# Performance work log

Hardware: AMD Instinct MI355X
Metric: run time of the kernel (lower is better)

## Reference

```python
import jax, jax.numpy as jnp
import numpy as np

EMB = 768  # SentenceT5 embedding dim; MLP input is 2*EMB


def setup_inputs() -> dict:
    key = jax.random.key(0)
    ks = jax.random.split(key, 9)
    B, S, D = 32, 32, 64
    num_doc = jax.random.randint(ks[0], (B,), 8, D + 1, dtype=jnp.int32)
    num_doc = num_doc.at[0].set(D)  # ensure max == padded dim (tf.reduce_max semantics)
    num_seg = jax.random.randint(ks[1], (B,), 4, S + 1, dtype=jnp.int32)
    num_seg = num_seg.at[0].set(S)
    doc_emb = jax.random.normal(ks[2], (B, D, EMB), jnp.float32)
    sum_emb = jax.random.normal(ks[3], (B, S, EMB), jnp.float32)
    # ragged .to_tensor() -> zero rows beyond per-sample length
    doc_emb = doc_emb * (jnp.arange(D)[None, :, None] < num_doc[:, None, None])
    sum_emb = sum_emb * (jnp.arange(S)[None, :, None] < num_seg[:, None, None])
    target_agg = jax.random.uniform(ks[4], (B,), jnp.float32)
    target_inst = jax.random.uniform(ks[5], (B, S), jnp.float32)
    w = lambda k, i, o: jax.random.normal(k, (i, o), jnp.float32) * 0.02
    W1 = w(ks[6], 2 * EMB, EMB)
    b1 = jnp.zeros((EMB,), jnp.float32)
    W2 = w(ks[7], EMB, EMB // 2)
    b2 = jnp.zeros((EMB // 2,), jnp.float32)
    W3 = w(ks[8], EMB // 2, 1)
    b3 = jnp.zeros((1,), jnp.float32)
    return dict(doc_emb=doc_emb, sum_emb=sum_emb, num_document_splits=num_doc,
                num_summary_segments=num_seg, target_agg_score=target_agg,
                target_instance_score=target_inst,
                W1=W1, b1=b1, W2=W2, b2=b2, W3=W3, b3=b3)


def _forward(doc_emb, sum_emb, num_doc, num_seg, W1, b1, W2, b2, W3, b3):
    B, D, E = doc_emb.shape
    S = sum_emb.shape[1]
    # concat([doc, seg]) @ W1 == doc @ W1[:E] + seg @ W1[E:]  (avoids materializing [B,S,D,2E])
    h_doc = jnp.einsum('bde,eh->bdh', doc_emb, W1[:E])   # [B,D,E]
    h_seg = jnp.einsum('bse,eh->bsh', sum_emb, W1[E:])   # [B,S,E]
    h1 = jax.nn.gelu(h_doc[:, None, :, :] + h_seg[:, :, None, :] + b1, approximate=False)  # [B,S,D,E]
    h2 = jax.nn.gelu(jnp.einsum('bsdh,hk->bsdk', h1, W2) + b2, approximate=False)          # [B,S,D,E/2]
    score = jax.nn.sigmoid(jnp.einsum('bsdk,ko->bsdo', h2, W3) + b3)[..., 0]               # [B,S,D]
    mask_d = (jnp.arange(D)[None, :] < num_doc[:, None]).astype(jnp.float32)               # [B,D]
    seg_max = jnp.max(mask_d[:, None, :] * score, axis=-1)                                 # [B,S]
    seg_w = jnp.where(num_seg > 10, 1.0, 100.0).astype(jnp.float32)                        # [B]
    pred = seg_w[:, None] * seg_max                                                        # [B,S]
    # cosine similarity prior (keras CosineSimilarity returns -cos)
    dn = doc_emb * jax.lax.rsqrt(jnp.maximum(jnp.sum(doc_emb * doc_emb, -1, keepdims=True), 1e-12))
    sn = sum_emb * jax.lax.rsqrt(jnp.maximum(jnp.sum(sum_emb * sum_emb, -1, keepdims=True), 1e-12))
    cs = -jnp.einsum('bde,bse->bsd', dn, sn)                                               # [B,S,D]
    dscos = jnp.max(mask_d[:, None, :] * (1.0 + cs) * 0.5, axis=-1)                        # [B,S]
    seg_mask = (jnp.arange(S)[None, :] < num_seg[:, None]).astype(jnp.float32)             # [B,S]
    diff = jnp.abs(dscos - pred) * seg_mask
    cos_prior = jnp.mean(jnp.sum(diff, axis=1) / num_seg.astype(jnp.float32))
    return pred, cos_prior


def reference(doc_emb, sum_emb, num_document_splits, num_summary_segments,
              target_agg_score, target_instance_score,
              W1, b1, W2, b2, W3, b3):
    B, S = target_instance_score.shape
    seg_mask = jnp.arange(S)[None, :] < num_summary_segments[:, None]
    # pad target instance scores with ones beyond per-sample length
    target_instance = jnp.where(seg_mask, target_instance_score, 1.0)
    pred, cos_prior = _forward(doc_emb, sum_emb, num_document_splits, num_summary_segments,
                               W1, b1, W2, b2, W3, b3)
    return (target_agg_score, target_instance, pred, num_summary_segments, cos_prior)
```

## Files before the change

### kernel.cpp

```cpp
#include <hip/hip_runtime.h>
#include <hip/hip_bf16.h>
#include <math.h>


typedef __bf16 bf16x8 __attribute__((ext_vector_type(8)));
typedef float f32x4 __attribute__((ext_vector_type(4)));

__device__ __forceinline__ unsigned short f2bf(float x) {
    unsigned int u = __float_as_uint(x);
    u = (u + 0x7fffu + ((u >> 16) & 1u)) >> 16;
    return (unsigned short)u;
}
__device__ __forceinline__ float exp2_fast(float x) {
    float r; asm("v_exp_f32 %0, %1" : "=v"(r) : "v"(x)); return r;
}
__device__ __forceinline__ float rcp_fast(float x) {
    float r; asm("v_rcp_f32 %0, %1" : "=v"(r) : "v"(x)); return r;
}
__device__ __forceinline__ unsigned int cvt_pk_bf16(float lo, float hi) {
    unsigned int r; asm("v_cvt_pk_bf16_f32 %0, %1, %2" : "=v"(r) : "v"(lo), "v"(hi)); return r;
}
__device__ __forceinline__ float gelu_fast(float x) {
    float t = x * fmaf(x * x, -0.10294325f, -2.3022081f);
    return x * rcp_fast(1.0f + exp2_fast(t));
}
__device__ __forceinline__ float sigmoid_fast(float x) {
    return rcp_fast(1.0f + exp2_fast(x * -1.4426950408889634f));
}
__device__ __forceinline__ float wave_sum(float v) {
    for (int o = 32; o; o >>= 1) v += __shfl_xor(v, o);
    return v;
}
__device__ __forceinline__ float wave_max(float v) {
    for (int o = 32; o; o >>= 1) v = fmaxf(v, __shfl_xor(v, o));
    return v;
}
__device__ __forceinline__ void soft_barrier() {
    __builtin_amdgcn_sched_barrier(0);
    asm volatile("s_waitcnt lgkmcnt(0)" ::: "memory");
    __builtin_amdgcn_s_barrier();
    __builtin_amdgcn_sched_barrier(0);
}
#define GLOAD_LDS16(GP, LP)                                                     \
    __builtin_amdgcn_global_load_lds(                                           \
        (const __attribute__((address_space(1))) unsigned int*)(GP),            \
        (__attribute__((address_space(3))) unsigned int*)(LP), 16, 0, 0)

__global__ __launch_bounds__(256) void prep_all(const float* __restrict__ W1,
                                                const float* __restrict__ W2,
                                                const float* __restrict__ doc,
                                                const float* __restrict__ sume,
                                                unsigned short* __restrict__ W1t,
                                                unsigned short* __restrict__ W2f,
                                                unsigned short* __restrict__ dnbf,
                                                unsigned short* __restrict__ snbf) {
    __shared__ __align__(16) char shbuf[49152];
    int id = blockIdx.x;
    int t = threadIdx.x;
    if (id < 288) {
        float (*tile)[65] = (float(*)[65])shbuf;
        int bx = id % 12, by = id / 12;
        int r0 = by * 64, c0 = bx * 64;
        #pragma unroll
        for (int p = 0; p < 16; ++p) {
            int r = p * 4 + (t >> 6), c = t & 63;
            tile[r][c] = W1[(r0 + r) * 768 + c0 + c];
        }
        __syncthreads();
        #pragma unroll
        for (int p = 0; p < 16; ++p) {
            int cc = p * 4 + (t >> 6), rr = t & 63;
            W1t[(c0 + cc) * 1536 + r0 + rr] = f2bf(tile[rr][cc]);
        }
    } else if (id < 300) {
        unsigned short* sh = (unsigned short*)shbuf;
        int kt = id - 288;
        #pragma unroll
        for (int p = 0; p < 96; ++p) {
            int u = p * 256 + t;
            int k = u / 384, n = u - k * 384;
            sh[u] = f2bf(W2[(kt * 64 + k) * 384 + n]);
        }
        __syncthreads();
        #pragma unroll
        for (int p = 0; p < 12; ++p) {
            int u = p * 256 + t;
            int lane = u & 63;
            int g = u >> 6;
            int ks = g / 24, fc = g - ks * 24;
            unsigned short tmp[8];
            #pragma unroll
            for (int j = 0; j < 8; ++j)
                tmp[j] = sh[(ks * 32 + (lane >> 4) * 8 + j) * 384 + fc * 16 + (lane & 15)];
            int ktks = kt * 2 + ks;
            *(uint4*)(W2f + ((ktks * 24 + fc) * 64 + lane) * 8) = *(uint4*)tmp;
        }
    } else {
        int row = (id - 300) * 4 + (t >> 6);
        int lane = t & 63;
        const float* p; unsigned short* dst;
        if (row < 2048) { p = doc + row * 768; dst = dnbf + row * 768; }
        else            { p = sume + (row - 2048) * 768; dst = snbf + (row - 2048) * 768; }
        const float* pp = p + lane * 12;
        float4 a0 = *(const float4*)(pp);
        float4 a1 = *(const float4*)(pp + 4);
        float4 a2 = *(const float4*)(pp + 8);
        float s = a0.x*a0.x + a0.y*a0.y + a0.z*a0.z + a0.w*a0.w
                + a1.x*a1.x + a1.y*a1.y + a1.z*a1.z + a1.w*a1.w
                + a2.x*a2.x + a2.y*a2.y + a2.z*a2.z + a2.w*a2.w;
        s = wave_sum(s);
        float r = rsqrtf(fmaxf(s, 1e-12f));
        unsigned short* dd = dst + lane * 12;
        dd[0]  = f2bf(a0.x * r); dd[1]  = f2bf(a0.y * r);
        dd[2]  = f2bf(a0.z * r); dd[3]  = f2bf(a0.w * r);
        dd[4]  = f2bf(a1.x * r); dd[5]  = f2bf(a1.y * r);
        dd[6]  = f2bf(a1.z * r); dd[7]  = f2bf(a1.w * r);
        dd[8]  = f2bf(a2.x * r); dd[9]  = f2bf(a2.y * r);
        dd[10] = f2bf(a2.z * r); dd[11] = f2bf(a2.w * r);
    }
}

__global__ __launch_bounds__(256) void gemm1(const float* __restrict__ doc,
                                             const float* __restrict__ sume,
                                             const unsigned short* __restrict__ W1t,
                                             const float* __restrict__ b1,
                                             unsigned short* __restrict__ hd,
                                             unsigned short* __restrict__ hs) {
    __shared__ __align__(16) unsigned short Asw[2][128 * 64];
    __shared__ __align__(16) unsigned short Bsw[2][64 * 64];
    int t = threadIdx.x;
    int row0 = blockIdx.y * 128, col0 = blockIdx.x * 64;
    bool is_doc = row0 < 2048;
    const float* A = is_doc ? (doc + row0 * 768) : (sume + (row0 - 2048) * 768);
    int kbase = is_doc ? 0 : 768;
    unsigned short* O = is_doc ? (hd + row0 * 768) : (hs + (row0 - 2048) * 768);

    int l = t & 63, w = t >> 6;
    int wr = w >> 1, wc = w & 1;
    int srow = t >> 3, sko = (t & 7) * 8;
    f32x4 acc[4][2];
    #pragma unroll
    for (int i = 0; i < 4; ++i)
        #pragma unroll
        for (int j = 0; j < 2; ++j) acc[i][j] = (f32x4)0.f;

    float4 fA0[4], fA1[4];
    bf16x8 bB[2];

#define G_LOAD(KT)                                                              \
    {                                                                           \
        _Pragma("unroll")                                                       \
        for (int p = 0; p < 4; ++p) {                                           \
            fA0[p] = *(const float4*)(A + (p * 32 + srow) * 768 + (KT) + sko);  \
            fA1[p] = *(const float4*)(A + (p * 32 + srow) * 768 + (KT) + sko + 4); \
        }                                                                       \
        _Pragma("unroll")                                                       \
        for (int p = 0; p < 2; ++p)                                             \
            bB[p] = *(const bf16x8*)(W1t + (col0 + p * 32 + srow) * 1536 + kbase + (KT) + sko); \
    }

#define G_STORE(BUF)                                                            \
    {                                                                           \
        char* AB = (char*)Asw[BUF];                                             \
        char* BB = (char*)Bsw[BUF];                                             \
        _Pragma("unroll")                                                       \
        for (int p = 0; p < 4; ++p) {                                           \
            uint4 v = make_uint4(cvt_pk_bf16(fA0[p].x, fA0[p].y),               \
                                 cvt_pk_bf16(fA0[p].z, fA0[p].w),               \
                                 cvt_pk_bf16(fA1[p].x, fA1[p].y),               \
                                 cvt_pk_bf16(fA1[p].z, fA1[p].w));              \
            int r = p * 32 + srow;                                              \
            int byte = (r * 128 + sko * 2) ^ ((r & 7) << 4);                    \
            *(uint4*)(AB + byte) = v;                                           \
        }                                                                       \
        _Pragma("unroll")                                                       \
        for (int p = 0; p < 2; ++p) {                                           \
            int r = p * 32 + srow;                                              \
            int byte = (r * 128 + sko * 2) ^ ((r & 7) << 4);                    \
            *(bf16x8*)(BB + byte) = bB[p];                                      \
        }                                                                       \
    }

    G_LOAD(0)
    G_STORE(0)
    G_LOAD(64)
    soft_barrier();

    #pragma unroll 1
    for (int i = 0; i < 12; ++i) {
        int cur = i & 1;
        const char* AR = (const char*)Asw[cur];
        const char* BR = (const char*)Bsw[cur];
        #pragma unroll
        for (int ks = 0; ks < 2; ++ks) {
            int koff = (ks * 32 + (l >> 4) * 8) * 2;
            bf16x8 af[4], bfr[2];
            #pragma unroll
            for (int fr = 0; fr < 4; ++fr) {
                int r = wr * 64 + fr * 16 + (l & 15);
                af[fr] = *(const bf16x8*)(AR + ((r * 128 + koff) ^ ((r & 7) << 4)));
            }
            #pragma unroll
            for (int fc = 0; fc < 2; ++fc) {
                int n = wc * 32 + fc * 16 + (l & 15);
                bfr[fc] = *(const bf16x8*)(BR + ((n * 128 + koff) ^ ((n & 7) << 4)));
            }
            #pragma unroll
            for (int fr = 0; fr < 4; ++fr)
                #pragma unroll
                for (int fc = 0; fc < 2; ++fc)
                    acc[fr][fc] = __builtin_amdgcn_mfma_f32_16x16x32_bf16(af[fr], bfr[fc], acc[fr][fc], 0, 0, 0);
        }
        if (i < 11) {
            G_STORE(cur ^ 1)
            if (i < 10) G_LOAD((i + 2) * 64)
        }
        soft_barrier();
    }
#undef G_LOAD
#undef G_STORE

    #pragma unroll
    for (int fr = 0; fr < 4; ++fr)
        #pragma unroll
        for (int fc = 0; fc < 2; ++fc) {
            int c = col0 + wc * 32 + fc * 16 + (l & 15);
            float badd = is_doc ? 0.0f : b1[c];
            #pragma unroll
            for (int j = 0; j < 4; ++j) {
                int r = wr * 64 + fr * 16 + (l >> 4) * 4 + j;
                O[r * 768 + c] = f2bf(acc[fr][fc][j] + badd);
            }
        }
}

__global__ __launch_bounds__(512) void score_mfma(
    const unsigned short* __restrict__ hd, const unsigned short* __restrict__ hs,
    const unsigned short* __restrict__ W2f,
    const float* __restrict__ b2, const float* __restrict__ W3,
    const float* __restrict__ b3, const int* __restrict__ ndoc,
    const int* __restrict__ nseg, const unsigned short* __restrict__ dnbf,
    const unsigned short* __restrict__ snbf, float* __restrict__ out,
    float* __restrict__ dscos)
{
    __shared__ __align__(16) char smem[90112];
    float* spart = (float*)smem;
    float* sred  = (float*)smem;

    int t = threadIdx.x;
    int l = t & 63, w = t >> 6;

    if (blockIdx.x < 32) {
        int b = (int)blockIdx.x;
        if (w < 4) {
            const unsigned short* sb = snbf + b * 32 * 768;
            const unsigned short* db = dnbf + b * 64 * 768;
            int arow = l & 15, ak = (l >> 4) * 8;
            int d0 = w * 16;
            f32x4 acc0 = (f32x4)0.f, acc1 = (f32x4)0.f;
            #pragma unroll
            for (int k = 0; k < 768; k += 32) {
                bf16x8 a0 = *(const bf16x8*)(sb + arow * 768 + k + ak);
                bf16x8 a1 = *(const bf16x8*)(sb + (16 + arow) * 768 + k + ak);
                bf16x8 bb = *(const bf16x8*)(db + (d0 + arow) * 768 + k + ak);
                acc0 = __builtin_amdgcn_mfma_f32_16x16x32_bf16(a0, bb, acc0, 0, 0, 0);
                acc1 = __builtin_amdgcn_mfma_f32_16x16x32_bf16(a1, bb, acc1, 0, 0, 0);
            }
            int nd = ndoc[b];
            int d = d0 + (l & 15);
            float v0[4], v1[4];
            #pragma unroll
            for (int j = 0; j < 4; ++j) {
                v0[j] = (d < nd) ? (1.f - acc0[j]) * 0.5f : 0.f;
                v1[j] = (d < nd) ? (1.f - acc1[j]) * 0.5f : 0.f;
            }
            #pragma unroll
            for (int o = 1; o < 16; o <<= 1) {
                #pragma unroll
                for (int j = 0; j < 4; ++j) {
                    v0[j] = fmaxf(v0[j], __shfl_xor(v0[j], o));
                    v1[j] = fmaxf(v1[j], __shfl_xor(v1[j], o));
                }
            }
            if ((l & 15) == 0) {
                int srw = (l >> 4) * 4;
                #pragma unroll
                for (int j = 0; j < 4; ++j) {
                    sred[w * 32 + srw + j] = v0[j];
                    sred[w * 32 + 16 + srw + j] = v1[j];
                }
            }
        }
        __syncthreads();
        if (t < 32)
            dscos[(int)blockIdx.x * 32 + t] = fmaxf(fmaxf(sred[t], sred[32 + t]),
                                                    fmaxf(sred[64 + t], sred[96 + t]));
        return;
    }

    int sb = (int)blockIdx.x - 32;
    int lb = (sb & 7) * 64 + (sb >> 3);
    int b = lb >> 4, sp = lb & 15;
    int s0 = sp * 2;
    int nd = ndoc[b], ns = nseg[b];
    int wr = w >> 2, wc = w & 3;

    f32x4 acc[4][6];
    #pragma unroll
    for (int i = 0; i < 4; ++i)
        #pragma unroll
        for (int j = 0; j < 6; ++j) acc[i][j] = (f32x4)0.f;

    int r = t >> 2;
    int k8 = t & 3;
    int d = r & 63, sl = r >> 6;
    const unsigned short* hdp = hd + (b * 64 + d) * 768 + k8 * 8;
    const unsigned short* hsp = hs + (b * 32 + s0 + sl) * 768 + k8 * 8;
    int abyte = ((r >> 4) * 1024 + k8 * 256 + (r & 15) * 16) ^ (k8 << 4);

    bf16x8 hdA, hsA, hdB, hsB;

#define A_LOAD(KT, HD8, HS8)                                                    \
    {                                                                           \
        HD8 = *(const bf16x8*)(hdp + (KT));                                     \
        HS8 = *(const bf16x8*)(hsp + (KT));                                     \
    }

#define B_STAGE(KC, BUF)                                                        \
    {                                                                           \
        _Pragma("unroll")                                                       \
        for (int q = 0; q < 3; ++q) {                                           \
            int fc = w * 3 + q;                                                 \
            const unsigned short* gsrc = W2f + (((KC) * 24 + fc) * 64 + l) * 8; \
            GLOAD_LDS16(gsrc, smem + 16384 + (BUF) * 24576 + fc * 1024);        \
        }                                                                       \
    }

#define A_STORE(HD8, HS8, BUF)                                                  \
    {                                                                           \
        const unsigned int* hu = (const unsigned int*)&HD8;                     \
        const unsigned int* su = (const unsigned int*)&HS8;                     \
        unsigned int au[4];                                                     \
        _Pragma("unroll")                                                       \
        for (int e = 0; e < 4; ++e) {                                           \
            float x0 = __uint_as_float(hu[e] << 16) + __uint_as_float(su[e] << 16); \
            float x1 = __uint_as_float(hu[e] & 0xffff0000u) + __uint_as_float(su[e] & 0xffff0000u); \
            au[e] = cvt_pk_bf16(gelu_fast(x0), gelu_fast(x1));                  \
        }                                                                       \
        *(uint4*)(smem + (BUF) * 8192 + abyte) = make_uint4(au[0], au[1], au[2], au[3]); \
    }

#define MFMA_PHASE(ABUF, BBUF)                                                  \
    {                                                                           \
        const char* AR = (const char*)smem + (ABUF) * 8192;                     \
        const char* BR = (const char*)smem + 16384 + (BBUF) * 24576;            \
        __builtin_amdgcn_s_setprio(1);                                          \
        bf16x8 af[4];                                                           \
        _Pragma("unroll")                                                       \
        for (int fr = 0; fr < 4; ++fr)                                          \
            af[fr] = *(const bf16x8*)(AR + (wr * 4 + fr) * 1024                 \
                                         + ((l * 16) ^ ((l >> 4) << 4)));       \
        _Pragma("unroll")                                                       \
        for (int i2 = 0; i2 < 6; ++i2) {                                        \
            bf16x8 bq = *(const bf16x8*)(BR + (wc * 6 + i2) * 1024 + l * 16);   \
            _Pragma("unroll")                                                   \
            for (int fr = 0; fr < 4; ++fr)                                      \
                acc[fr][i2] = __builtin_amdgcn_mfma_f32_16x16x32_bf16(af[fr], bq, acc[fr][i2], 0, 0, 0); \
        }                                                                       \
        __builtin_amdgcn_s_setprio(0);                                          \
    }

#define SYNC_CNT()                                                              \
    __builtin_amdgcn_sched_barrier(0);                                          \
    asm volatile("s_waitcnt vmcnt(5) lgkmcnt(0)" ::: "memory");                 \
    __builtin_amdgcn_s_barrier();                                               \
    __builtin_amdgcn_sched_barrier(0);

#define K_ITER(J, HDL, HSL, HDS, HSS)                                           \
    {                                                                           \
        int i_ = base + (J);                                                    \
        if (i_ < 22) {                                                          \
            B_STAGE(i_ + 2, ((J) + 2) % 3)                                      \
            A_LOAD((i_ + 2) * 32, HDL, HSL)                                     \
        }                                                                       \
        MFMA_PHASE((J) & 1, (J) % 3)                                            \
        if (i_ < 23) A_STORE(HDS, HSS, ((J) + 1) & 1)                           \
        SYNC_CNT()                                                              \
    }

    A_LOAD(0, hdA, hsA)
    B_STAGE(0, 0)
    B_STAGE(1, 1)
    A_STORE(hdA, hsA, 0)
    A_LOAD(32, hdB, hsB)
    SYNC_CNT()

    #pragma unroll 1
    for (int base = 0; base < 24; base += 6) {
        K_ITER(0, hdA, hsA, hdB, hsB)
        K_ITER(1, hdB, hsB, hdA, hsA)
        K_ITER(2, hdA, hsA, hdB, hsB)
        K_ITER(3, hdB, hsB, hdA, hsA)
        K_ITER(4, hdA, hsA, hdB, hsB)
        K_ITER(5, hdB, hsB, hdA, hsA)
    }
#undef A_LOAD
#undef B_STAGE
#undef A_STORE
#undef MFMA_PHASE
#undef SYNC_CNT
#undef K_ITER

    float b2v[6], w3v[6];
    #pragma unroll
    for (int i2 = 0; i2 < 6; ++i2) {
        int col = wc * 96 + i2 * 16 + (l & 15);
        b2v[i2] = b2[col];
        w3v[i2] = W3[col];
    }
    __syncthreads();
    #pragma unroll
    for (int fr = 0; fr < 4; ++fr) {
        #pragma unroll
        for (int j = 0; j < 4; ++j) {
            float pr = 0.f;
            #pragma unroll
            for (int i2 = 0; i2 < 6; ++i2)
                pr += gelu_fast(acc[fr][i2][j] + b2v[i2]) * w3v[i2];
            pr += __shfl_xor(pr, 1);
            pr += __shfl_xor(pr, 2);
            pr += __shfl_xor(pr, 4);
            pr += __shfl_xor(pr, 8);
            if ((l & 15) == 0)
                spart[wc * 128 + wr * 64 + fr * 16 + (l >> 4) * 4 + j] = pr;
        }
    }
    __syncthreads();
    if (t < 128) {
        int row = t;
        float v = spart[row] + spart[128 + row] + spart[256 + row] + spart[384 + row] + b3[0];
        float sc = sigmoid_fast(v);
        int dd = row & 63, sl2 = row >> 6;
        float m = (dd < nd) ? sc : 0.f;
        m = wave_max(m);
        if ((t & 63) == 0) {
            float segw = (ns > 10) ? 1.f : 100.f;
            out[1056 + b * 32 + s0 + sl2] = segw * m;
        }
    }
}

__global__ __launch_bounds__(1024) void finish_k(const float* __restrict__ agg,
                                                 const float* __restrict__ tinst,
                                                 const int* __restrict__ nseg,
                                                 const float* __restrict__ dscos,
                                                 float* __restrict__ out) {
    __shared__ float red[16];
    int t = threadIdx.x, lane = t & 63, w = t >> 6;
    int b = t >> 5, s = t & 31;
    int ns = nseg[b];
    out[32 + t] = (s < ns) ? tinst[t] : 1.0f;
    if (t < 32) {
        out[t] = agg[t];
        out[2080 + t] = (float)nseg[t];
    }
    float pred = out[1056 + t];
    float v = (s < ns) ? fabsf(dscos[t] - pred) / (float)ns : 0.f;
    v = wave_sum(v);
    if (lane == 0) red[w] = v;
    __syncthreads();
    if (w == 0) {
        float x = (lane < 16) ? red[lane] : 0.f;
        x = wave_sum(x);
        if (lane == 0) out[2112] = x * (1.f / 32.f);
    }
}

extern "C" void kernel_launch(void* const* d_in, const int* in_sizes, int n_in,
                              void* d_out, int out_size, void* d_ws, size_t ws_size,
                              hipStream_t stream) {
    const float* doc   = (const float*)d_in[0];
    const float* sume  = (const float*)d_in[1];
    const int*   ndoc  = (const int*)d_in[2];
    const int*   nseg  = (const int*)d_in[3];
    const float* agg   = (const float*)d_in[4];
    const float* tinst = (const float*)d_in[5];
    const float* W1    = (const float*)d_in[6];
    const float* b1    = (const float*)d_in[7];
    const float* W2    = (const float*)d_in[8];
    const float* b2    = (const float*)d_in[9];
    const float* W3    = (const float*)d_in[10];
    const float* b3    = (const float*)d_in[11];
    float* out = (float*)d_out;
    char* ws = (char*)d_ws;

    unsigned short* hd   = (unsigned short*)(ws);
    unsigned short* hs   = (unsigned short*)(ws + 3145728);
    unsigned short* W1t  = (unsigned short*)(ws + 4718592);
    unsigned short* W2f  = (unsigned short*)(ws + 7077888);
    unsigned short* dnbf = (unsigned short*)(ws + 7667712);
    unsigned short* snbf = (unsigned short*)(ws + 10813440);
    float* dscos = (float*)(ws + 12386304);

    prep_all<<<1068, 256, 0, stream>>>(W1, W2, doc, sume, W1t, W2f, dnbf, snbf);
    gemm1<<<dim3(12, 24), 256, 0, stream>>>(doc, sume, W1t, b1, hd, hs);
    score_mfma<<<544, 512, 0, stream>>>(hd, hs, W2f, b2, W3, b3, ndoc, nseg,
                                        dnbf, snbf, out, dscos);
    finish_k<<<1, 1024, 0, stream>>>(agg, tinst, nseg, dscos, out);
}
```

Measured before the change: 99.20 us.

## Shrink score tile to one segment per 256-thread block and peel loop tail

The score kernel now uses 256-thread blocks that each handle a single (batch, segment) pair over 64 doc rows, instead of 512-thread blocks covering two segments, which doubles the grid to 1056 blocks. Each wave now covers 96 output columns for all 64 rows, so each block stages twice as much W2 per wave with a smaller A tile. The K loop drops its per-iteration bounds checks by peeling the last iterations into an explicit epilogue, and the wait count changes to match. The smaller LDS footprint could let more blocks share a CU, but W2 is reloaded from global memory per segment, twice as often as before, which raises memory traffic.

```diff
diff --git a/kernel.cpp b/kernel.cpp
--- a/kernel.cpp
+++ b/kernel.cpp
@@ -234,7 +234,7 @@
         }
 }
 
-__global__ __launch_bounds__(512) void score_mfma(
+__global__ __launch_bounds__(256) void score_mfma(
     const unsigned short* __restrict__ hd, const unsigned short* __restrict__ hs,
     const unsigned short* __restrict__ W2f,
     const float* __restrict__ b2, const float* __restrict__ W3,
@@ -243,7 +243,7 @@
     const unsigned short* __restrict__ snbf, float* __restrict__ out,
     float* __restrict__ dscos)
 {
-    __shared__ __align__(16) char smem[90112];
+    __shared__ __align__(16) char smem[81920];
     float* spart = (float*)smem;
     float* sred  = (float*)smem;
 
@@ -252,7 +252,7 @@
 
     if (blockIdx.x < 32) {
         int b = (int)blockIdx.x;
-        if (w < 4) {
+        {
             const unsigned short* sb = snbf + b * 32 * 768;
             const unsigned short* db = dnbf + b * 64 * 768;
             int arow = l & 15, ak = (l >> 4) * 8;
@@ -299,11 +299,9 @@
     }
 
     int sb = (int)blockIdx.x - 32;
-    int lb = (sb & 7) * 64 + (sb >> 3);
-    int b = lb >> 4, sp = lb & 15;
-    int s0 = sp * 2;
+    int lb = (sb & 7) * 128 + (sb >> 3);
+    int b = lb >> 5, s = lb & 31;
     int nd = ndoc[b], ns = nseg[b];
-    int wr = w >> 2, wc = w & 3;
 
     f32x4 acc[4][6];
     #pragma unroll
@@ -311,12 +309,11 @@
         #pragma unroll
         for (int j = 0; j < 6; ++j) acc[i][j] = (f32x4)0.f;
 
-    int r = t >> 2;
+    int d = t >> 2;
     int k8 = t & 3;
-    int d = r & 63, sl = r >> 6;
     const unsigned short* hdp = hd + (b * 64 + d) * 768 + k8 * 8;
-    const unsigned short* hsp = hs + (b * 32 + s0 + sl) * 768 + k8 * 8;
-    int abyte = ((r >> 4) * 1024 + k8 * 256 + (r & 15) * 16) ^ (k8 << 4);
+    const unsigned short* hsp = hs + (b * 32 + s) * 768 + k8 * 8;
+    int abyte = (d >> 4) * 1024 + (((d & 15) | (k8 << 4)) * 16);
 
     bf16x8 hdA, hsA, hdB, hsB;
 
@@ -329,10 +326,10 @@
 #define B_STAGE(KC, BUF)                                                        \
     {                                                                           \
         _Pragma("unroll")                                                       \
-        for (int q = 0; q < 3; ++q) {                                           \
-            int fc = w * 3 + q;                                                 \
+        for (int q = 0; q < 6; ++q) {                                           \
+            int fc = w * 6 + q;                                                 \
             const unsigned short* gsrc = W2f + (((KC) * 24 + fc) * 64 + l) * 8; \
-            GLOAD_LDS16(gsrc, smem + 16384 + (BUF) * 24576 + fc * 1024);        \
+            GLOAD_LDS16(gsrc, smem + 8192 + (BUF) * 24576 + fc * 1024);         \
         }                                                                       \
     }
 
@@ -347,22 +344,21 @@
             float x1 = __uint_as_float(hu[e] & 0xffff0000u) + __uint_as_float(su[e] & 0xffff0000u); \
             au[e] = cvt_pk_bf16(gelu_fast(x0), gelu_fast(x1));                  \
         }                                                                       \
-        *(uint4*)(smem + (BUF) * 8192 + abyte) = make_uint4(au[0], au[1], au[2], au[3]); \
+        *(uint4*)(smem + (BUF) * 4096 + abyte) = make_uint4(au[0], au[1], au[2], au[3]); \
     }
 
 #define MFMA_PHASE(ABUF, BBUF)                                                  \
     {                                                                           \
-        const char* AR = (const char*)smem + (ABUF) * 8192;                     \
-        const char* BR = (const char*)smem + 16384 + (BBUF) * 24576;            \
+        const char* AR = (const char*)smem + (ABUF) * 4096;                     \
+        const char* BR = (const char*)smem + 8192 + (BBUF) * 24576;             \
         __builtin_amdgcn_s_setprio(1);                                          \
         bf16x8 af[4];                                                           \
         _Pragma("unroll")                                                       \
         for (int fr = 0; fr < 4; ++fr)                                          \
-            af[fr] = *(const bf16x8*)(AR + (wr * 4 + fr) * 1024                 \
-                                         + ((l * 16) ^ ((l >> 4) << 4)));       \
+            af[fr] = *(const bf16x8*)(AR + fr * 1024 + l * 16);                 \
         _Pragma("unroll")                                                       \
         for (int i2 = 0; i2 < 6; ++i2) {                                        \
-            bf16x8 bq = *(const bf16x8*)(BR + (wc * 6 + i2) * 1024 + l * 16);   \
+            bf16x8 bq = *(const bf16x8*)(BR + (w * 6 + i2) * 1024 + l * 16);    \
             _Pragma("unroll")                                                   \
             for (int fr = 0; fr < 4; ++fr)                                      \
                 acc[fr][i2] = __builtin_amdgcn_mfma_f32_16x16x32_bf16(af[fr], bq, acc[fr][i2], 0, 0, 0); \
@@ -370,33 +366,30 @@
         __builtin_amdgcn_s_setprio(0);                                          \
     }
 
-#define SYNC_CNT()                                                              \
+#define SYNC_CNT(CNTSTR)                                                        \
     __builtin_amdgcn_sched_barrier(0);                                          \
-    asm volatile("s_waitcnt vmcnt(5) lgkmcnt(0)" ::: "memory");                 \
+    asm volatile(CNTSTR ::: "memory");                                          \
     __builtin_amdgcn_s_barrier();                                               \
     __builtin_amdgcn_sched_barrier(0);
 
 #define K_ITER(J, HDL, HSL, HDS, HSS)                                           \
     {                                                                           \
-        int i_ = base + (J);                                                    \
-        if (i_ < 22) {                                                          \
-            B_STAGE(i_ + 2, ((J) + 2) % 3)                                      \
-            A_LOAD((i_ + 2) * 32, HDL, HSL)                                     \
-        }                                                                       \
+        B_STAGE(base + (J) + 2, ((J) + 2) % 3)                                  \
+        A_LOAD((base + (J) + 2) * 32, HDL, HSL)                                 \
         MFMA_PHASE((J) & 1, (J) % 3)                                            \
-        if (i_ < 23) A_STORE(HDS, HSS, ((J) + 1) & 1)                           \
-        SYNC_CNT()                                                              \
-    }
-
-    A_LOAD(0, hdA, hsA)
+        A_STORE(HDS, HSS, ((J) + 1) & 1)                                        \
+        SYNC_CNT("s_waitcnt vmcnt(8) lgkmcnt(0)")                               \
+    }
+
     B_STAGE(0, 0)
     B_STAGE(1, 1)
+    A_LOAD(0, hdA, hsA)
     A_STORE(hdA, hsA, 0)
     A_LOAD(32, hdB, hsB)
-    SYNC_CNT()
+    SYNC_CNT("s_waitcnt vmcnt(8) lgkmcnt(0)")
 
     #pragma unroll 1
-    for (int base = 0; base < 24; base += 6) {
+    for (int base = 0; base < 18; base += 6) {
         K_ITER(0, hdA, hsA, hdB, hsB)
         K_ITER(1, hdB, hsB, hdA, hsA)
         K_ITER(2, hdA, hsA, hdB, hsB)
@@ -404,6 +397,17 @@
         K_ITER(4, hdA, hsA, hdB, hsB)
         K_ITER(5, hdB, hsB, hdA, hsA)
     }
+    {
+        int base = 18;
+        K_ITER(0, hdA, hsA, hdB, hsB)
+        K_ITER(1, hdB, hsB, hdA, hsA)
+        K_ITER(2, hdA, hsA, hdB, hsB)
+        K_ITER(3, hdB, hsB, hdA, hsA)
+    }
+    MFMA_PHASE(0, 1)
+    A_STORE(hdB, hsB, 1)
+    SYNC_CNT("s_waitcnt vmcnt(0) lgkmcnt(0)")
+    MFMA_PHASE(1, 2)
 #undef A_LOAD
 #undef B_STAGE
 #undef A_STORE
@@ -414,7 +418,7 @@
     float b2v[6], w3v[6];
     #pragma unroll
     for (int i2 = 0; i2 < 6; ++i2) {
-        int col = wc * 96 + i2 * 16 + (l & 15);
+        int col = w * 96 + i2 * 16 + (l & 15);
         b2v[i2] = b2[col];
         w3v[i2] = W3[col];
     }
@@ -432,20 +436,19 @@
             pr += __shfl_xor(pr, 4);
             pr += __shfl_xor(pr, 8);
             if ((l & 15) == 0)
-                spart[wc * 128 + wr * 64 + fr * 16 + (l >> 4) * 4 + j] = pr;
+                spart[w * 64 + fr * 16 + (l >> 4) * 4 + j] = pr;
         }
     }
     __syncthreads();
-    if (t < 128) {
+    if (t < 64) {
         int row = t;
-        float v = spart[row] + spart[128 + row] + spart[256 + row] + spart[384 + row] + b3[0];
+        float v = spart[row] + spart[64 + row] + spart[128 + row] + spart[192 + row] + b3[0];
         float sc = sigmoid_fast(v);
-        int dd = row & 63, sl2 = row >> 6;
-        float m = (dd < nd) ? sc : 0.f;
+        float m = (row < nd) ? sc : 0.f;
         m = wave_max(m);
-        if ((t & 63) == 0) {
+        if (t == 0) {
             float segw = (ns > 10) ? 1.f : 100.f;
-            out[1056 + b * 32 + s0 + sl2] = segw * m;
+            out[1056 + b * 32 + s] = segw * m;
         }
     }
 }
@@ -504,7 +507,7 @@
 
     prep_all<<<1068, 256, 0, stream>>>(W1, W2, doc, sume, W1t, W2f, dnbf, snbf);
     gemm1<<<dim3(12, 24), 256, 0, stream>>>(doc, sume, W1t, b1, hd, hs);
-    score_mfma<<<544, 512, 0, stream>>>(hd, hs, W2f, b2, W3, b3, ndoc, nseg,
-                                        dnbf, snbf, out, dscos);
+    score_mfma<<<1056, 256, 0, stream>>>(hd, hs, W2f, b2, W3, b3, ndoc, nseg,
+                                         dnbf, snbf, out, dscos);
     finish_k<<<1, 1024, 0, stream>>>(agg, tinst, nseg, dscos, out);
 }
```

New measurement: 104.1 us. 1.05x slower.
